# Kernel tuning notes

Hardware: AMD Instinct MI355X
Metric: run time of the kernel (lower is better)

## Reference

```python
import jax, jax.numpy as jnp
import numpy as np
import math

B, L, D, H, DK, DFF = 4, 1024, 1024, 16, 64, 4096
NUM_BUCKETS, MAX_DIST = 32, 128


def _relative_position_bucket(rel):
    # bidirectional T5 bucketing; rel = memory_pos - context_pos
    nb = NUM_BUCKETS // 2
    n = -rel
    ret = (n < 0).astype(jnp.int32) * nb
    n = jnp.abs(n)
    max_exact = nb // 2
    is_small = n < max_exact
    val_if_large = max_exact + (
        jnp.log(jnp.maximum(n, 1).astype(jnp.float32) / max_exact)
        / math.log(MAX_DIST / max_exact)
        * (nb - max_exact)
    ).astype(jnp.int32)
    val_if_large = jnp.minimum(val_if_large, nb - 1)
    return ret + jnp.where(is_small, n.astype(jnp.int32), val_if_large)


def t5_layernorm(x, w, eps):
    # no mean subtraction, no bias (T5 style)
    var = jnp.mean(jnp.square(x.astype(jnp.float32)), axis=-1, keepdims=True)
    return w * (x / jnp.sqrt(var + eps))


def setup_inputs() -> dict:
    key = jax.random.key(0)
    ks = jax.random.split(key, 12)
    inp = {
        "src": jax.random.normal(ks[0], (B, L, D), dtype=jnp.float32),
        "enc_position": jnp.broadcast_to(jnp.arange(L, dtype=jnp.int32), (B, L)),
        "ln1_w": jnp.ones((D,), jnp.float32),
        "wq": jax.random.normal(ks[1], (H * DK, D), jnp.float32) * (D * DK) ** -0.5,
        "bq": jnp.zeros((H * DK,), jnp.float32),
        "wk": jax.random.normal(ks[2], (H * DK, D), jnp.float32) * D ** -0.5,
        "bk": jnp.zeros((H * DK,), jnp.float32),
        "wv": jax.random.normal(ks[3], (H * DK, D), jnp.float32) * D ** -0.5,
        "bv": jnp.zeros((H * DK,), jnp.float32),
        "fc_w": jax.random.normal(ks[4], (D, H * DK), jnp.float32) * (H * DK) ** -0.5,
        "fc_b": jnp.zeros((D,), jnp.float32),
        "rel_bias": jax.random.normal(ks[5], (NUM_BUCKETS, H), jnp.float32) * 0.02,
        "ln2_w": jnp.ones((D,), jnp.float32),
        "wi": jax.random.normal(ks[6], (DFF, D), jnp.float32) * D ** -0.5,
        "wo": jax.random.normal(ks[7], (D, DFF), jnp.float32) * DFF ** -0.5,
    }
    return inp


def reference(src, enc_position, ln1_w, wq, bq, wk, bk, wv, bv, fc_w, fc_b,
              rel_bias, ln2_w, wi, wo):
    b, l, d = src.shape
    temp = DK ** 0.5

    # --- Multi-head self attention (pre-LN, T5 relative bias) ---
    proj = t5_layernorm(src, ln1_w, 1e-12)
    q = (proj @ wq.T + bq).reshape(b, l, H, DK).transpose(0, 2, 1, 3)  # [b,h,l,dk]
    k = (proj @ wk.T + bk).reshape(b, l, H, DK).transpose(0, 2, 1, 3)
    v = (proj @ wv.T + bv).reshape(b, l, H, DK).transpose(0, 2, 1, 3)

    # relative position bias: [b, h, l_q, l_k]
    rel = enc_position[:, None, :] - enc_position[:, :, None]  # mem - ctx
    bucket = _relative_position_bucket(rel)                    # [b, l, l]
    position_bias = rel_bias[bucket].transpose(0, 3, 1, 2)     # [b, h, l, l]

    scores = jnp.einsum("bhqd,bhkd->bhqk", q / temp, k) + position_bias
    attn = jax.nn.softmax(scores, axis=-1)                     # dropout = eval no-op
    ctx = jnp.einsum("bhqk,bhkd->bhqd", attn, v)
    ctx = ctx.transpose(0, 2, 1, 3).reshape(b, l, H * DK)
    attn_out = ctx @ fc_w.T + fc_b + src                       # residual
    attn_sum = jnp.sum(attn, axis=1)                           # [b, l, l]

    # --- Position-wise FFN (pre-LN, gelu, no biases) ---
    nx = t5_layernorm(attn_out, ln2_w, 1e-6)
    h = jax.nn.gelu(nx @ wi.T, approximate=False)
    out = attn_out + h @ wo.T
    return out, attn_sum, position_bias
```

## Files before the change

### kernel.cpp

```cpp
#include <hip/hip_runtime.h>
#include <hip/hip_bf16.h>
#include <math.h>

typedef __attribute__((ext_vector_type(8))) short short8;
typedef __attribute__((ext_vector_type(4))) float f32x4;
typedef unsigned short u16;

#define L2E 1.44269504088896340736f

__device__ __forceinline__ u16 f2bf(float f) {
  union { float f; unsigned u; } x; x.f = f;
  unsigned r = x.u + 0x7fffu + ((x.u >> 16) & 1u);
  return (u16)(r >> 16);
}

__device__ __forceinline__ void gload16(const void* g, void* l) {
  auto gp = reinterpret_cast<const __attribute__((address_space(1))) void*>(
      reinterpret_cast<uintptr_t>(g));
  auto lp = reinterpret_cast<__attribute__((address_space(3))) void*>(
      reinterpret_cast<uintptr_t>(l));
  __builtin_amdgcn_global_load_lds(gp, lp, 16, 0, 0);
}

__device__ __forceinline__ int xcd_swz(int flat, int nwg) {
  return (flat & 7) * (nwg >> 3) + (flat >> 3);
}

__device__ __forceinline__ int bucket_fn(int rel) {
  int n = -rel;
  int ret = 0;
  if (n < 0) { ret = 16; n = -n; }
  if (n < 8) return ret + n;
  int e = 31 - __clz(n);
  unsigned nn = (unsigned)n * (unsigned)n;
  int f = 2 * e + ((nn >= (1u << (2 * e + 1))) ? 1 : 0) - 6;
  int val = 8 + f;
  if (val > 15) val = 15;
  return ret + val;
}

__global__ __launch_bounds__(256) void prep(
    const float* __restrict__ wq, const float* __restrict__ wk,
    const float* __restrict__ wv, const float* __restrict__ fcw,
    const float* __restrict__ wi, const float* __restrict__ wo,
    const float* __restrict__ bq, const float* __restrict__ bk,
    const float* __restrict__ bv, const float* __restrict__ rel_bias,
    u16* __restrict__ wqb, u16* __restrict__ wkb, u16* __restrict__ wvb,
    u16* __restrict__ fcwb, u16* __restrict__ wib, u16* __restrict__ wob,
    float* __restrict__ fb, float* __restrict__ tab) {
  const int blk = blockIdx.x, t = threadIdx.x;
  if (blk < 12288) {
    const float* s; u16* d; int rel;
    if (blk < 1024)      { s = wq;  d = wqb;  rel = blk; }
    else if (blk < 2048) { s = wk;  d = wkb;  rel = blk - 1024; }
    else if (blk < 3072) { s = wv;  d = wvb;  rel = blk - 2048; }
    else if (blk < 4096) { s = fcw; d = fcwb; rel = blk - 3072; }
    else if (blk < 8192) { s = wi;  d = wib;  rel = blk - 4096; }
    else                 { s = wo;  d = wob;  rel = blk - 8192; }
    const int i = (rel * 256 + t) * 4;
    float4 v = *(const float4*)&s[i];
    d[i + 0] = f2bf(v.x); d[i + 1] = f2bf(v.y);
    d[i + 2] = f2bf(v.z); d[i + 3] = f2bf(v.w);
  } else if (blk < 12300) {
    const int i = (blk - 12288) * 256 + t;
    fb[i] = i < 1024 ? bq[i] : (i < 2048 ? bk[i - 1024] : bv[i - 2048]);
  } else {
    const int idx = (blk - 12300) * 256 + t;
    const int h = idx >> 11;
    const int rel = (idx & 2047) - 1024;
    tab[idx] = rel_bias[bucket_fn(rel) * 16 + h];
  }
}

__global__ __launch_bounds__(256) void write_pb(const float* __restrict__ tab,
                                                float* __restrict__ pb) {
  const int i = blockIdx.x, h = blockIdx.y, t = threadIdx.x;
  __shared__ float tabs[2048];
  ((float4*)tabs)[t]       = ((const float4*)(tab + h * 2048))[t];
  ((float4*)tabs)[t + 256] = ((const float4*)(tab + h * 2048))[t + 256];
  __syncthreads();
  const int j = t * 4;
  float4 o;
  o.x = tabs[j + 0 - i + 1024];
  o.y = tabs[j + 1 - i + 1024];
  o.z = tabs[j + 2 - i + 1024];
  o.w = tabs[j + 3 - i + 1024];
#pragma unroll
  for (int b = 0; b < 4; b++)
    *(float4*)&pb[(((size_t)(b * 16 + h)) * 1024 + i) * 1024 + j] = o;
}

__global__ __launch_bounds__(256) void t5_ln(const float* __restrict__ x,
                                             const float* __restrict__ wgt,
                                             float eps, u16* __restrict__ out) {
  const int row = blockIdx.x, t = threadIdx.x;
  const float4 v = ((const float4*)(x + (size_t)row * 1024))[t];
  float ss = v.x * v.x + v.y * v.y + v.z * v.z + v.w * v.w;
#pragma unroll
  for (int off = 1; off < 64; off <<= 1) ss += __shfl_xor(ss, off, 64);
  __shared__ float red[4];
  if ((t & 63) == 0) red[t >> 6] = ss;
  __syncthreads();
  float tot = red[0] + red[1] + red[2] + red[3];
  float inv = 1.0f / sqrtf(tot * (1.0f / 1024.0f) + eps);
  const float4 wv = ((const float4*)wgt)[t];
  u16* o = out + (size_t)row * 1024 + t * 4;
  o[0] = f2bf(v.x * inv * wv.x);
  o[1] = f2bf(v.y * inv * wv.y);
  o[2] = f2bf(v.z * inv * wv.z);
  o[3] = f2bf(v.w * inv * wv.w);
}

__global__ __launch_bounds__(256) void transpose_v(const u16* __restrict__ v,
                                                   u16* __restrict__ vt) {
  __shared__ u16 T[64][72];
  const int bh = blockIdx.y;
  const int l0 = blockIdx.x * 64;
  const int t = threadIdx.x;
  const int sr = t >> 3, sc = (t & 7) * 8;
  const u16* vb = v + (size_t)bh * 65536;
  *(short8*)&T[sr][sc]      = *(const short8*)&vb[(size_t)(l0 + sr) * 64 + sc];
  *(short8*)&T[sr + 32][sc] = *(const short8*)&vb[(size_t)(l0 + sr + 32) * 64 + sc];
  __syncthreads();
  u16* vtb = vt + (size_t)bh * 65536;
  short8 o0, o1;
#pragma unroll
  for (int u = 0; u < 8; u++) {
    ((u16*)&o0)[u] = T[sc + u][sr];
    ((u16*)&o1)[u] = T[sc + u][sr + 32];
  }
  *(short8*)&vtb[(size_t)sr * 1024 + l0 + sc]        = o0;
  *(short8*)&vtb[(size_t)(sr + 32) * 1024 + l0 + sc] = o1;
}

template<int MODE>
__global__ __launch_bounds__(256, 3) void gemm_nt(
    const u16* __restrict__ A, const u16* __restrict__ Bw,
    int M, int N, int K,
    const float* __restrict__ bias, const float* __restrict__ res,
    float scale, float* __restrict__ outF, u16* __restrict__ outB) {
  __shared__ u16 As[3][4096];
  __shared__ u16 Bs[3][4096];
  const int t = threadIdx.x;
  const int w = t >> 6, lane = t & 63;
  const int wr = w >> 1, wc = w & 1;
  const int g = lane >> 4, lc = lane & 15;

  const int nwg = gridDim.x * gridDim.y;
  const int flat = xcd_swz(blockIdx.y * gridDim.x + blockIdx.x, nwg);
  const int bx = flat % gridDim.x, by = flat / gridDim.x;
  const int m0 = by * 128, n0 = bx * 128;

  const int srow = w * 16 + (lane >> 2);
  const int sc8  = (lane & 3) ^ ((srow >> 1) & 3);
  const u16* Ag = &A[(size_t)(m0 + srow) * K + sc8 * 8];
  const u16* Bg = &Bw[(size_t)(n0 + srow) * K + sc8 * 8];
  const size_t row64 = (size_t)64 * K;
  const int swz = (lc >> 1) & 3;

  const int NT = K >> 5;
  f32x4 acc[4][4] = {};

  auto stage = [&](int buf, int tt) {
    const int k0 = tt << 5;
    u16* lA = &As[buf][w * 512];
    u16* lB = &Bs[buf][w * 512];
    gload16(Ag + k0, lA);
    gload16(Ag + row64 + k0, lA + 2048);
    gload16(Bg + k0, lB);
    gload16(Bg + row64 + k0, lB + 2048);
  };

  stage(0, 0);
  stage(1, 1);

  for (int tt = 0; tt < NT; tt++) {
    const int cur = tt % 3;
    if (tt < NT - 1) {
      asm volatile("s_waitcnt vmcnt(4)" ::: "memory");
    } else {
      asm volatile("s_waitcnt vmcnt(0)" ::: "memory");
    }
    __builtin_amdgcn_s_barrier();
    short8 af[4], bf[4];
#pragma unroll
    for (int mi = 0; mi < 4; mi++)
      af[mi] = *(short8*)&As[cur][(wr * 64 + mi * 16 + lc) * 32 + (g ^ swz) * 8];
#pragma unroll
    for (int ni = 0; ni < 4; ni++)
      bf[ni] = *(short8*)&Bs[cur][(wc * 64 + ni * 16 + lc) * 32 + (g ^ swz) * 8];
    if (tt + 2 < NT) stage((tt + 2) % 3, tt + 2);
#pragma unroll
    for (int mi = 0; mi < 4; mi++)
#pragma unroll
      for (int ni = 0; ni < 4; ni++)
        acc[mi][ni] = __builtin_amdgcn_mfma_f32_16x16x32_bf16(af[mi], bf[ni], acc[mi][ni], 0, 0, 0);
  }

  u16* Es = &As[0][0];
  __syncthreads();
#pragma unroll
  for (int mi = 0; mi < 4; mi++) {
#pragma unroll
    for (int ni = 0; ni < 4; ni++) {
#pragma unroll
      for (int r = 0; r < 4; r++) {
        const int col = n0 + wc * 64 + ni * 16 + lc;
        float v = acc[mi][ni][r];
        if (MODE == 0) {
          v = (v + bias[col]) * ((col >> 10) == 0 ? scale : 1.0f);
        } else {
          v = 0.5f * v * (1.0f + erff(v * 0.70710678118654752440f));
        }
        Es[wr * 2048 + (g * 4 + r) * 128 + wc * 64 + ni * 16 + lc] = f2bf(v);
      }
    }
    __syncthreads();
    {
      const int rr = t >> 3;
      const int wr2 = rr >> 4, r16 = rr & 15;
      const int cc = (t & 7) * 16;
      short8 o0 = *(short8*)&Es[wr2 * 2048 + r16 * 128 + cc];
      short8 o1 = *(short8*)&Es[wr2 * 2048 + r16 * 128 + cc + 8];
      const int row = m0 + wr2 * 64 + mi * 16 + r16;
      if (MODE == 0) {
        const int col0 = n0 + cc;
        const int which = col0 >> 10, c = col0 & 1023;
        const int hh = c >> 6, dk = c & 63;
        const int b = row >> 10, pos = row & 1023;
        u16* dst = outB + (size_t)which * 4194304 +
                   (((size_t)(b * 16 + hh)) * 1024 + pos) * 64 + dk;
        *(short8*)dst = o0;
        *(short8*)(dst + 8) = o1;
      } else {
        u16* dst = outB + (size_t)row * (size_t)N + n0 + cc;
        *(short8*)dst = o0;
        *(short8*)(dst + 8) = o1;
      }
    }
    __syncthreads();
  }
}

template<int MODE>
__global__ __launch_bounds__(256, 4) void gemm_nt64(
    const u16* __restrict__ A, const u16* __restrict__ Bw,
    int M, int N, int K,
    const float* __restrict__ bias, const float* __restrict__ res,
    float* __restrict__ outF) {
  __shared__ u16 As[3][2048];
  __shared__ u16 Bs[3][4096];
  const int t = threadIdx.x;
  const int w = t >> 6, lane = t & 63;
  const int wr = w >> 1, wc = w & 1;
  const int g = lane >> 4, lc = lane & 15;

  const int nwg = gridDim.x * gridDim.y;
  const int flat = xcd_swz(blockIdx.y * gridDim.x + blockIdx.x, nwg);
  const int bx = flat % gridDim.x, by = flat / gridDim.x;
  const int m0 = by * 64, n0 = bx * 128;

  const int srow = w * 16 + (lane >> 2);
  const int sc8  = (lane & 3) ^ ((srow >> 1) & 3);
  const u16* Ag = &A[(size_t)(m0 + srow) * K + sc8 * 8];
  const u16* Bg = &Bw[(size_t)(n0 + srow) * K + sc8 * 8];
  const size_t row64 = (size_t)64 * K;
  const int swz = (lc >> 1) & 3;

  const int NT = K >> 5;
  f32x4 acc[2][4] = {};

  auto stage = [&](int buf, int tt) {
    const int k0 = tt << 5;
    gload16(Ag + k0, &As[buf][w * 512]);
    gload16(Bg + k0, &Bs[buf][w * 512]);
    gload16(Bg + row64 + k0, &Bs[buf][w * 512 + 2048]);
  };

  stage(0, 0);
  stage(1, 1);

  for (int tt = 0; tt < NT; tt++) {
    const int cur = tt % 3;
    if (tt < NT - 1) {
      asm volatile("s_waitcnt vmcnt(3)" ::: "memory");
    } else {
      asm volatile("s_waitcnt vmcnt(0)" ::: "memory");
    }
    __builtin_amdgcn_s_barrier();
    short8 af[2], bf[4];
#pragma unroll
    for (int mi = 0; mi < 2; mi++)
      af[mi] = *(short8*)&As[cur][(wr * 32 + mi * 16 + lc) * 32 + (g ^ swz) * 8];
#pragma unroll
    for (int ni = 0; ni < 4; ni++)
      bf[ni] = *(short8*)&Bs[cur][(wc * 64 + ni * 16 + lc) * 32 + (g ^ swz) * 8];
    if (tt + 2 < NT) stage((tt + 2) % 3, tt + 2);
#pragma unroll
    for (int mi = 0; mi < 2; mi++)
#pragma unroll
      for (int ni = 0; ni < 4; ni++)
        acc[mi][ni] = __builtin_amdgcn_mfma_f32_16x16x32_bf16(af[mi], bf[ni], acc[mi][ni], 0, 0, 0);
  }

#pragma unroll
  for (int mi = 0; mi < 2; mi++) {
#pragma unroll
    for (int ni = 0; ni < 4; ni++) {
#pragma unroll
      for (int r = 0; r < 4; r++) {
        const int row = m0 + wr * 32 + mi * 16 + g * 4 + r;
        const int col = n0 + wc * 64 + ni * 16 + lc;
        float v = acc[mi][ni][r];
        if (MODE == 1) {
          v += bias[col] + res[(size_t)row * 1024 + col];
        } else {
          v += res[(size_t)row * 1024 + col];
        }
        outF[(size_t)row * 1024 + col] = v;
      }
    }
  }
}

__global__ __launch_bounds__(256) void attn_kernel(
    const u16* __restrict__ q, const u16* __restrict__ k,
    const u16* __restrict__ vt, const float* __restrict__ tab,
    u16* __restrict__ ctx, float* __restrict__ ml) {
  const int flat = xcd_swz(blockIdx.y * 16 + blockIdx.x, 1024);
  const int bh = flat / 16;
  const int i0 = (flat % 16) * 64;
  const int h = bh & 15, b = bh >> 4;
  const int t = threadIdx.x, w = t >> 6, lane = t & 63;
  const int g = lane >> 4, lc = lane & 15;
  const int sr = t >> 3;
  const int swc = ((t & 7) ^ (sr & 7)) * 8;
  const int sc = (t & 7) * 8;

  __shared__ u16 Ks[2][64][64];
  __shared__ u16 Vts[2][64][64];
  __shared__ u16 P[4][16][64];
  __shared__ float tabs[2048];

  const u16* qb  = q + (size_t)bh * 65536;
  const u16* kb  = k + (size_t)bh * 65536;
  const u16* vtb = vt + (size_t)bh * 65536;

  {
    float4 t0 = ((const float4*)(tab + h * 2048))[t];
    float4 t1 = ((const float4*)(tab + h * 2048))[t + 256];
    t0.x *= L2E; t0.y *= L2E; t0.z *= L2E; t0.w *= L2E;
    t1.x *= L2E; t1.y *= L2E; t1.z *= L2E; t1.w *= L2E;
    ((float4*)tabs)[t]       = t0;
    ((float4*)tabs)[t + 256] = t1;
  }

  const short8 aq0 = *(const short8*)&qb[(size_t)(i0 + w * 16 + lc) * 64 + g * 8];
  const short8 aq1 = *(const short8*)&qb[(size_t)(i0 + w * 16 + lc) * 64 + 32 + g * 8];

  {
    short8 ka = *(const short8*)&kb[(size_t)sr * 64 + sc];
    short8 kc = *(const short8*)&kb[(size_t)(sr + 32) * 64 + sc];
    short8 va = *(const short8*)&vtb[(size_t)sr * 1024 + sc];
    short8 vc = *(const short8*)&vtb[(size_t)(sr + 32) * 1024 + sc];
    *(short8*)&Ks[0][sr][swc]       = ka;
    *(short8*)&Ks[0][sr + 32][swc]  = kc;
    *(short8*)&Vts[0][sr][swc]      = va;
    *(short8*)&Vts[0][sr + 32][swc] = vc;
  }
  __syncthreads();

  const int rx = lc & 7;
  const int ibase = 1024 - i0 - (w * 16 + g * 4) + lc;

  float m_r[4] = {-INFINITY, -INFINITY, -INFINITY, -INFINITY};
  float l_r[4] = {0.f, 0.f, 0.f, 0.f};
  f32x4 cacc[4] = {};

  for (int tt = 0; tt < 16; tt++) {
    const int buf = tt & 1;
    const int j0 = tt * 64;

    short8 nka, nkc, nva, nvc;
    if (tt < 15) {
      const int jn = j0 + 64;
      nka = *(const short8*)&kb[(size_t)(jn + sr) * 64 + sc];
      nkc = *(const short8*)&kb[(size_t)(jn + sr + 32) * 64 + sc];
      nva = *(const short8*)&vtb[(size_t)sr * 1024 + jn + sc];
      nvc = *(const short8*)&vtb[(size_t)(sr + 32) * 1024 + jn + sc];
    }

    f32x4 s[4] = {};
#pragma unroll
    for (int ni = 0; ni < 4; ni++) {
      short8 b0 = *(short8*)&Ks[buf][ni * 16 + lc][(g ^ rx) * 8];
      short8 b1 = *(short8*)&Ks[buf][ni * 16 + lc][((4 + g) ^ rx) * 8];
      s[ni] = __builtin_amdgcn_mfma_f32_16x16x32_bf16(aq0, b0, s[ni], 0, 0, 0);
      s[ni] = __builtin_amdgcn_mfma_f32_16x16x32_bf16(aq1, b1, s[ni], 0, 0, 0);
    }
#pragma unroll
    for (int ni = 0; ni < 4; ni++)
#pragma unroll
      for (int r = 0; r < 4; r++)
        s[ni][r] += tabs[ibase + j0 + ni * 16 - r];

#pragma unroll
    for (int r = 0; r < 4; r++) {
      float tm = fmaxf(fmaxf(s[0][r], s[1][r]), fmaxf(s[2][r], s[3][r]));
#pragma unroll
      for (int off = 1; off < 16; off <<= 1) tm = fmaxf(tm, __shfl_xor(tm, off, 64));
      const float mn = fmaxf(m_r[r], tm);
      const float scl = __builtin_amdgcn_exp2f(m_r[r] - mn);
      float rs = 0.f;
#pragma unroll
      for (int ni = 0; ni < 4; ni++) {
        float p = __builtin_amdgcn_exp2f(s[ni][r] - mn);
        s[ni][r] = p;
        rs += p;
      }
#pragma unroll
      for (int off = 1; off < 16; off <<= 1) rs += __shfl_xor(rs, off, 64);
      l_r[r] = l_r[r] * scl + rs;
      m_r[r] = mn;
#pragma unroll
      for (int d = 0; d < 4; d++) cacc[d][r] *= scl;
    }

#pragma unroll
    for (int ni = 0; ni < 4; ni++)
#pragma unroll
      for (int r = 0; r < 4; r++) {
        const int prow = g * 4 + r;
        P[w][prow][(((ni * 2 + (lc >> 3)) ^ (prow & 7)) << 3) | (lc & 7)] = f2bf(s[ni][r]);
      }

    short8 ap0 = *(short8*)&P[w][lc][(g ^ rx) * 8];
    short8 ap1 = *(short8*)&P[w][lc][((4 + g) ^ rx) * 8];
#pragma unroll
    for (int d = 0; d < 4; d++) {
      short8 bv0 = *(short8*)&Vts[buf][d * 16 + lc][(g ^ rx) * 8];
      short8 bv1 = *(short8*)&Vts[buf][d * 16 + lc][((4 + g) ^ rx) * 8];
      cacc[d] = __builtin_amdgcn_mfma_f32_16x16x32_bf16(ap0, bv0, cacc[d], 0, 0, 0);
      cacc[d] = __builtin_amdgcn_mfma_f32_16x16x32_bf16(ap1, bv1, cacc[d], 0, 0, 0);
    }

    if (tt < 15) {
      *(short8*)&Ks[buf ^ 1][sr][swc]       = nka;
      *(short8*)&Ks[buf ^ 1][sr + 32][swc]  = nkc;
      *(short8*)&Vts[buf ^ 1][sr][swc]      = nva;
      *(short8*)&Vts[buf ^ 1][sr + 32][swc] = nvc;
    }
    __syncthreads();
  }

  float inv[4];
#pragma unroll
  for (int r = 0; r < 4; r++) inv[r] = 1.0f / l_r[r];
#pragma unroll
  for (int d = 0; d < 4; d++)
#pragma unroll
    for (int r = 0; r < 4; r++) {
      const int pos = i0 + w * 16 + g * 4 + r;
      ctx[((size_t)b * 1024 + pos) * 1024 + h * 64 + d * 16 + lc] = f2bf(cacc[d][r] * inv[r]);
    }
  if (lc == 0) {
#pragma unroll
    for (int r = 0; r < 4; r++) {
      const int i = i0 + w * 16 + g * 4 + r;
      ml[(size_t)bh * 1024 + i] = m_r[r];
      ml[65536 + (size_t)bh * 1024 + i] = l_r[r];
    }
  }
}

__global__ __launch_bounds__(256) void attn_sum_kernel(
    const u16* __restrict__ q, const u16* __restrict__ k,
    const float* __restrict__ tab, const float* __restrict__ ml,
    float* __restrict__ asum) {
  const int flat = xcd_swz(((blockIdx.z * 16 + blockIdx.y) * 16) + blockIdx.x, 1024);
  const int j0 = (flat % 16) * 64;
  const int i0 = ((flat / 16) % 16) * 64;
  const int b = flat / 256;
  const int t = threadIdx.x, w = t >> 6, lane = t & 63;
  const int g = lane >> 4, lc = lane & 15;
  const int sr = t >> 3;
  const int swc = ((t & 7) ^ (sr & 7)) * 8;
  const int sc = (t & 7) * 8;
  const int rx = lc & 7;
  __shared__ u16 Ks[64][64];
  __shared__ float tabs[128];

  f32x4 acc[4] = {};

  for (int h = 0; h < 16; h++) {
    const int bh = b * 16 + h;
    __syncthreads();
    const u16* kb = k + (size_t)bh * 65536;
    *(short8*)&Ks[sr][swc]      = *(const short8*)&kb[(size_t)(j0 + sr) * 64 + sc];
    *(short8*)&Ks[sr + 32][swc] = *(const short8*)&kb[(size_t)(j0 + sr + 32) * 64 + sc];
    if (t < 127) tabs[t] = tab[h * 2048 + (j0 - i0 - 63 + t) + 1024] * L2E;
    __syncthreads();
    const u16* qb = q + (size_t)bh * 65536;
    short8 aq0 = *(const short8*)&qb[(size_t)(i0 + w * 16 + lc) * 64 + g * 8];
    short8 aq1 = *(const short8*)&qb[(size_t)(i0 + w * 16 + lc) * 64 + 32 + g * 8];
    f32x4 s[4] = {};
#pragma unroll
    for (int ni = 0; ni < 4; ni++) {
      short8 b0 = *(short8*)&Ks[ni * 16 + lc][(g ^ rx) * 8];
      short8 b1 = *(short8*)&Ks[ni * 16 + lc][((4 + g) ^ rx) * 8];
      s[ni] = __builtin_amdgcn_mfma_f32_16x16x32_bf16(aq0, b0, s[ni], 0, 0, 0);
      s[ni] = __builtin_amdgcn_mfma_f32_16x16x32_bf16(aq1, b1, s[ni], 0, 0, 0);
    }
    float mm[4], li[4];
#pragma unroll
    for (int r = 0; r < 4; r++) {
      const int i = i0 + w * 16 + g * 4 + r;
      mm[r] = ml[(size_t)bh * 1024 + i];
      li[r] = 1.0f / ml[65536 + (size_t)bh * 1024 + i];
    }
#pragma unroll
    for (int ni = 0; ni < 4; ni++)
#pragma unroll
      for (int r = 0; r < 4; r++) {
        float sv = s[ni][r] + tabs[ni * 16 + lc - w * 16 - g * 4 - r + 63];
        acc[ni][r] += __builtin_amdgcn_exp2f(sv - mm[r]) * li[r];
      }
  }
#pragma unroll
  for (int ni = 0; ni < 4; ni++)
#pragma unroll
    for (int r = 0; r < 4; r++) {
      const int i = i0 + w * 16 + g * 4 + r;
      asum[((size_t)b * 1024 + i) * 1024 + j0 + ni * 16 + lc] = acc[ni][r];
    }
}

extern "C" void kernel_launch(void* const* d_in, const int* in_sizes, int n_in,
                              void* d_out, int out_size, void* d_ws, size_t ws_size,
                              hipStream_t stream) {
  const float* src      = (const float*)d_in[0];
  const float* ln1_w    = (const float*)d_in[2];
  const float* wq       = (const float*)d_in[3];
  const float* bq       = (const float*)d_in[4];
  const float* wk       = (const float*)d_in[5];
  const float* bk       = (const float*)d_in[6];
  const float* wv       = (const float*)d_in[7];
  const float* bv       = (const float*)d_in[8];
  const float* fc_w     = (const float*)d_in[9];
  const float* fc_b     = (const float*)d_in[10];
  const float* rel_bias = (const float*)d_in[11];
  const float* ln2_w    = (const float*)d_in[12];
  const float* wi       = (const float*)d_in[13];
  const float* wo       = (const float*)d_in[14];

  const size_t MB = 1u << 20;
  char* ws = (char*)d_ws;
  u16* wq_b   = (u16*)(ws + 0 * MB);
  u16* wk_b   = (u16*)(ws + 2 * MB);
  u16* wv_b   = (u16*)(ws + 4 * MB);
  u16* fcw_b  = (u16*)(ws + 6 * MB);
  u16* wi_b   = (u16*)(ws + 8 * MB);
  u16* wo_b   = (u16*)(ws + 16 * MB);
  u16* proj_b = (u16*)(ws + 24 * MB);
  u16* q_b    = (u16*)(ws + 32 * MB);
  u16* k_b    = (u16*)(ws + 40 * MB);
  u16* v_b    = (u16*)(ws + 48 * MB);
  u16* vt_b   = (u16*)(ws + 56 * MB);
  u16* h_b    = (u16*)(ws + 32 * MB);
  u16* ctx_b  = (u16*)(ws + 64 * MB);
  float* attn_out = (float*)(ws + 72 * MB);
  float* ml   = (float*)(ws + 88 * MB);
  float* tab  = (float*)(ws + 88 * MB + 512 * 1024);
  float* fb   = (float*)(ws + 90 * MB);

  float* outF = (float*)d_out;
  float* asum = outF + 4194304;
  float* pb   = outF + 8388608;

  prep<<<12428, 256, 0, stream>>>(wq, wk, wv, fc_w, wi, wo, bq, bk, bv, rel_bias,
                                  wq_b, wk_b, wv_b, fcw_b, wi_b, wo_b, fb, tab);

  write_pb<<<dim3(1024, 16), 256, 0, stream>>>(tab, pb);

  t5_ln<<<4096, 256, 0, stream>>>(src, ln1_w, 1e-12f, proj_b);

  gemm_nt<0><<<dim3(24, 32), 256, 0, stream>>>(proj_b, wq_b, 4096, 3072, 1024, fb, nullptr,
                                               0.125f * L2E, nullptr, q_b);

  transpose_v<<<dim3(16, 64), 256, 0, stream>>>(v_b, vt_b);
  attn_kernel<<<dim3(16, 64), 256, 0, stream>>>(q_b, k_b, vt_b, tab, ctx_b, ml);
  attn_sum_kernel<<<dim3(16, 16, 4), 256, 0, stream>>>(q_b, k_b, tab, ml, asum);

  gemm_nt64<1><<<dim3(8, 64), 256, 0, stream>>>(ctx_b, fcw_b, 4096, 1024, 1024, fc_b, src, attn_out);

  t5_ln<<<4096, 256, 0, stream>>>(attn_out, ln2_w, 1e-6f, proj_b);

  gemm_nt<2><<<dim3(32, 32), 256, 0, stream>>>(proj_b, wi_b, 4096, 4096, 1024, nullptr, nullptr,
                                               1.0f, nullptr, h_b);
  gemm_nt64<3><<<dim3(8, 64), 256, 0, stream>>>(h_b, wo_b, 4096, 1024, 4096, nullptr, attn_out, outF);
}
```

Before: 351.3 us.

## Use 256x256 tile GEMM with 512 threads for FFN up-projection with GELU

Adds a new GEMM kernel using 256x256 output tiles, 8 waves of 512 threads, a triple-buffered LDS pipeline and a fused erf-GELU epilogue, and routes the FFN up-projection through it instead of the generic gemm_nt. Larger tiles raise arithmetic intensity and cut global/L2 traffic per FLOP. The cost is only 256 workgroups, about one wave over the CUs, so tail and occupancy effects may matter, and the epilogue serialises the stores with many barriers.

```diff
diff --git a/kernel.cpp b/kernel.cpp
--- a/kernel.cpp
+++ b/kernel.cpp
@@ -242,6 +242,98 @@
   }
 }
 
+__global__ __launch_bounds__(512, 2) void gemm256_gelu(
+    const u16* __restrict__ A, const u16* __restrict__ Bw,
+    int M, int N, int K, u16* __restrict__ outB) {
+  __shared__ u16 As[3][8192];
+  __shared__ u16 Bs[3][8192];
+  const int t = threadIdx.x;
+  const int w = t >> 6, lane = t & 63;
+  const int wrm = w >> 2, wcn = w & 3;
+  const int g = lane >> 4, lc = lane & 15;
+
+  const int nwg = gridDim.x * gridDim.y;
+  const int flat = xcd_swz(blockIdx.y * gridDim.x + blockIdx.x, nwg);
+  const int bx = flat % gridDim.x, by = flat / gridDim.x;
+  const int m0 = by * 256, n0 = bx * 256;
+
+  const int srow = w * 16 + (lane >> 2);
+  const int sc8  = (lane & 3) ^ ((srow >> 1) & 3);
+  const u16* Ag = &A[(size_t)(m0 + srow) * K + sc8 * 8];
+  const u16* Bg = &Bw[(size_t)(n0 + srow) * K + sc8 * 8];
+  const size_t row128 = (size_t)128 * K;
+  const int swz = (lc >> 1) & 3;
+
+  const int NT = K >> 5;
+  f32x4 acc[8][4] = {};
+
+  auto stage = [&](int buf, int tt) {
+    const int k0 = tt << 5;
+    u16* lA = &As[buf][w * 512];
+    u16* lB = &Bs[buf][w * 512];
+    gload16(Ag + k0, lA);
+    gload16(Ag + row128 + k0, lA + 4096);
+    gload16(Bg + k0, lB);
+    gload16(Bg + row128 + k0, lB + 4096);
+  };
+
+  stage(0, 0);
+  stage(1, 1);
+
+  for (int tt = 0; tt < NT; tt++) {
+    const int cur = tt % 3;
+    if (tt < NT - 1) {
+      asm volatile("s_waitcnt vmcnt(4)" ::: "memory");
+    } else {
+      asm volatile("s_waitcnt vmcnt(0)" ::: "memory");
+    }
+    __builtin_amdgcn_s_barrier();
+    short8 af[8], bf[4];
+#pragma unroll
+    for (int mi = 0; mi < 8; mi++)
+      af[mi] = *(short8*)&As[cur][(wrm * 128 + mi * 16 + lc) * 32 + (g ^ swz) * 8];
+#pragma unroll
+    for (int ni = 0; ni < 4; ni++)
+      bf[ni] = *(short8*)&Bs[cur][(wcn * 64 + ni * 16 + lc) * 32 + (g ^ swz) * 8];
+    if (tt + 2 < NT) stage((tt + 2) % 3, tt + 2);
+    __builtin_amdgcn_s_setprio(1);
+#pragma unroll
+    for (int mi = 0; mi < 8; mi++)
+#pragma unroll
+      for (int ni = 0; ni < 4; ni++)
+        acc[mi][ni] = __builtin_amdgcn_mfma_f32_16x16x32_bf16(af[mi], bf[ni], acc[mi][ni], 0, 0, 0);
+    __builtin_amdgcn_s_setprio(0);
+  }
+
+  u16* Es = &As[0][0];
+  __syncthreads();
+#pragma unroll
+  for (int mi = 0; mi < 8; mi++) {
+#pragma unroll
+    for (int ni = 0; ni < 4; ni++) {
+#pragma unroll
+      for (int r = 0; r < 4; r++) {
+        float v = acc[mi][ni][r];
+        v = 0.5f * v * (1.0f + erff(v * 0.70710678118654752440f));
+        Es[(wrm * 16 + g * 4 + r) * 256 + wcn * 64 + ni * 16 + lc] = f2bf(v);
+      }
+    }
+    __syncthreads();
+    {
+      const int rr = t >> 4;
+      const int wr2 = rr >> 4, r16 = rr & 15;
+      const int cc = (t & 15) * 16;
+      short8 o0 = *(short8*)&Es[(wr2 * 16 + r16) * 256 + cc];
+      short8 o1 = *(short8*)&Es[(wr2 * 16 + r16) * 256 + cc + 8];
+      const int row = m0 + wr2 * 128 + mi * 16 + r16;
+      u16* dst = outB + (size_t)row * (size_t)N + n0 + cc;
+      *(short8*)dst = o0;
+      *(short8*)(dst + 8) = o1;
+    }
+    __syncthreads();
+  }
+}
+
 template<int MODE>
 __global__ __launch_bounds__(256, 4) void gemm_nt64(
     const u16* __restrict__ A, const u16* __restrict__ Bw,
@@ -595,7 +687,6 @@
 
   t5_ln<<<4096, 256, 0, stream>>>(attn_out, ln2_w, 1e-6f, proj_b);
 
-  gemm_nt<2><<<dim3(32, 32), 256, 0, stream>>>(proj_b, wi_b, 4096, 4096, 1024, nullptr, nullptr,
-                                               1.0f, nullptr, h_b);
+  gemm256_gelu<<<dim3(16, 16), 512, 0, stream>>>(proj_b, wi_b, 4096, 4096, 1024, h_b);
   gemm_nt64<3><<<dim3(8, 64), 256, 0, stream>>>(h_b, wo_b, 4096, 1024, 4096, nullptr, attn_out, outF);
 }
```

After: 360.4 us. +2.6%, slower.
